# Kernel optimization log

Measured on AMD Instinct MI355X. Metric: run time of the kernel, lower is better.

Reference implementation:

```python
import jax, jax.numpy as jnp
import numpy as np

LN_EPS = 1e-5

def _layernorm(x, g, b):
    mu = jnp.mean(x, axis=-1, keepdims=True)
    var = jnp.mean(jnp.square(x - mu), axis=-1, keepdims=True)
    return (x - mu) * jax.lax.rsqrt(var + LN_EPS) * g + b

def setup_inputs() -> dict:
    key = jax.random.key(0)
    ks = jax.random.split(key, 12)
    B, S, E = 8, 4096, 512
    H, DK = 64, 8          # d_k = E // H = 8 qubits per head
    NQ_FFN, FFN = 8, 2048
    TWO_PI = 2.0 * np.pi
    x = jax.random.normal(ks[0], (B, S, E), dtype=jnp.float32)
    # trainable RX phases per attention head/wire; trainable RY phases for FFN qubits
    theta_attn = jax.random.uniform(ks[1], (H, DK), dtype=jnp.float32, maxval=TWO_PI)
    theta_ffn = jax.random.uniform(ks[2], (NQ_FFN,), dtype=jnp.float32, maxval=TWO_PI)
    s_e = 1.0 / np.sqrt(E)
    W_comb = jax.random.uniform(ks[3], (E, E), dtype=jnp.float32, minval=-s_e, maxval=s_e)
    b_comb = jax.random.uniform(ks[4], (E,), dtype=jnp.float32, minval=-s_e, maxval=s_e)
    s_q = 1.0 / np.sqrt(NQ_FFN)
    W1 = jax.random.uniform(ks[5], (FFN, NQ_FFN), dtype=jnp.float32, minval=-s_q, maxval=s_q)
    b1 = jax.random.uniform(ks[6], (FFN,), dtype=jnp.float32, minval=-s_q, maxval=s_q)
    s_f = 1.0 / np.sqrt(FFN)
    W2 = jax.random.uniform(ks[7], (E, FFN), dtype=jnp.float32, minval=-s_f, maxval=s_f)
    b2 = jax.random.uniform(ks[8], (E,), dtype=jnp.float32, minval=-s_f, maxval=s_f)
    ln1_g = jnp.ones((E,), jnp.float32); ln1_b = jnp.zeros((E,), jnp.float32)
    ln2_g = jnp.ones((E,), jnp.float32); ln2_b = jnp.zeros((E,), jnp.float32)
    return {"x": x, "theta_attn": theta_attn, "W_comb": W_comb, "b_comb": b_comb,
            "ln1_g": ln1_g, "ln1_b": ln1_b, "theta_ffn": theta_ffn,
            "W1": W1, "b1": b1, "W2": W2, "b2": b2, "ln2_g": ln2_g, "ln2_b": ln2_b}

def reference(x, theta_attn, W_comb, b_comb, ln1_g, ln1_b, theta_ffn, W1, b1, W2, b2, ln2_g, ln2_b):
    B, S, E = x.shape
    H, DK = theta_attn.shape
    NQ = theta_ffn.shape[0]
    # Quantum attention heads: RX(x) then RX(theta) on |0> per wire -> <Z> = cos(x+theta)
    q = jnp.cos(x.reshape(B, S, H, DK) + theta_attn)  # [B,S,H,DK]
    attn_out = jnp.einsum('bse,fe->bsf', q.reshape(B, S, E), W_comb) + b_comb
    x1 = _layernorm(x + attn_out, ln1_g, ln1_b)
    # Quantum FFN layer: RY(x) then RY(theta) -> <Z> = cos(x+theta), first NQ features only
    fq = jnp.cos(x1[..., :NQ] + theta_ffn)            # [B,S,NQ]
    h = jax.nn.relu(jnp.einsum('bsq,fq->bsf', fq, W1) + b1)
    ffn_out = jnp.einsum('bsf,ef->bse', h, W2) + b2
    return _layernorm(x1 + ffn_out, ln2_g, ln2_b)
```

## Files before the change

kernel.cpp:

```cpp
#include <hip/hip_runtime.h>
#include <stdint.h>

typedef unsigned short u16;
typedef __bf16 bf16x8 __attribute__((ext_vector_type(8)));
typedef float f32x4 __attribute__((ext_vector_type(4)));

#define AS1(p) ((const __attribute__((address_space(1))) void*)(p))
#define AS3(p) ((__attribute__((address_space(3))) void*)(p))

__device__ __forceinline__ float b2f(u16 v){
    union { unsigned u; float f; } x; x.u = ((unsigned)v) << 16; return x.f;
}
__device__ __forceinline__ u16 f2b(float f){
    union { float f; unsigned u; } x; x.f = f;
    unsigned r = x.u + 0x7FFFu + ((x.u >> 16) & 1u);
    return (u16)(r >> 16);
}

__global__ __launch_bounds__(256) void probe_kernel(
    const u16* p0,const u16* p1,const u16* p2,const u16* p3,const u16* p4,
    const u16* p5,const u16* p6,const u16* p7,const u16* p8,const u16* p9,
    const u16* p10,const u16* p11,const u16* p12,
    int n0,int n1,int n2,int n3,int n4,int n5,int n6,int n7,int n8,int n9,
    int n10,int n11,int n12, int* flags)
{
    const u16* p; int n;
    switch (blockIdx.x) {
        case 0: p=p0; n=n0; break;   case 1: p=p1; n=n1; break;
        case 2: p=p2; n=n2; break;   case 3: p=p3; n=n3; break;
        case 4: p=p4; n=n4; break;   case 5: p=p5; n=n5; break;
        case 6: p=p6; n=n6; break;   case 7: p=p7; n=n7; break;
        case 8: p=p8; n=n8; break;   case 9: p=p9; n=n9; break;
        case 10: p=p10; n=n10; break; case 11: p=p11; n=n11; break;
        default: p=p12; n=n12; break;
    }
    int pairs = n >> 1; if (pairs > 2048) pairs = 2048;
    int strong = 0, znz = 0, tot = 0;
    for (int k = threadIdx.x; k < pairs; k += 256) {
        u16 lo = p[2*k], hi = p[2*k+1];
        int eh = (hi >> 7) & 0xFF;
        int el = (lo >> 7) & 0xFF;
        if (eh >= 0xF0 || (eh >= 1 && eh <= 0x40)) strong = 1;
        if (el >= 0xF0 || (el >= 1 && el <= 0x40)) strong = 1;
        if (lo == 0 && hi != 0) znz++;
        tot++;
    }
    __shared__ int ss, sz, st;
    if (threadIdx.x == 0) { ss = 0; sz = 0; st = 0; }
    __syncthreads();
    if (strong) atomicOr(&ss, 1);
    if (znz) atomicAdd(&sz, znz);
    atomicAdd(&st, tot);
    __syncthreads();
    if (threadIdx.x == 0) {
        flags[blockIdx.x] = (ss || (2 * sz > st)) ? 1 : 0;
        if (blockIdx.x == 0) flags[15] = 0;
    }
}

__global__ __launch_bounds__(256) void convert_kernel(
    const void* sWc, const void* sW2, const void* sW1,
    const void* sTa, const void* sBc, const void* sG1, const void* sB1l,
    const void* sTf, const void* sB1, const void* sB2, const void* sG2, const void* sB2l,
    u16* wbase, const int* flags)
{
    int b = blockIdx.x;
    const void* src; u16* dst; int n, fi, lb, tof32 = 0;
    if (b < 128)      { src=sWc; dst=wbase;          n=262144;  fi=2;  lb=b; }
    else if (b < 640) { src=sW2; dst=wbase+262144;   n=1048576; fi=9;  lb=b-128; }
    else if (b >= 643 && b < 651) { src=sW1; dst=wbase+1312256; n=16384; fi=7; lb=b-643; }
    else {
        lb = 0;
        switch (b) {
            case 640: src=sTa;  dst=wbase+1310720; n=512;  fi=1;  break;
            case 641: src=sBc;  dst=wbase+1311232; n=512;  fi=3;  break;
            case 642: src=sB2;  dst=wbase+1311744; n=512;  fi=10; break;
            case 651: src=sB1;  dst=wbase+1328640; n=2048; fi=8;  break;
            case 652: src=sG1;  dst=wbase+1330688; n=512;  fi=4;  break;
            case 653: src=sB1l; dst=wbase+1331200; n=512;  fi=5;  break;
            case 654: src=sG2;  dst=wbase+1331712; n=512;  fi=11; break;
            case 655: src=sB2l; dst=wbase+1332224; n=512;  fi=12; break;
            default:  src=sTf;  dst=wbase+1332736; n=8;    fi=6;  tof32=1; break;
        }
    }
    int i = lb * 256 + threadIdx.x;
    if (i * 8 >= n) return;
    if (tof32) {
        float* fd = (float*)dst;
        if (flags[fi]) {
            const float4* s = (const float4*)src;
            ((float4*)fd)[i*2] = s[i*2]; ((float4*)fd)[i*2+1] = s[i*2+1];
        } else {
            union { uint4 v; u16 h[8]; } sb;
            sb.v = ((const uint4*)src)[i];
            #pragma unroll
            for (int j = 0; j < 8; j++) fd[i*8+j] = b2f(sb.h[j]);
        }
        return;
    }
    if (flags[fi]) {
        const float4* s = (const float4*)src;
        float4 a = s[i*2], c = s[i*2+1];
        union { uint4 v; u16 h[8]; } o;
        o.h[0]=f2b(a.x); o.h[1]=f2b(a.y); o.h[2]=f2b(a.z); o.h[3]=f2b(a.w);
        o.h[4]=f2b(c.x); o.h[5]=f2b(c.y); o.h[6]=f2b(c.z); o.h[7]=f2b(c.w);
        ((uint4*)dst)[i] = o.v;
    } else {
        ((uint4*)dst)[i] = ((const uint4*)src)[i];
    }
}

__global__ __launch_bounds__(256) void qgen_kernel(
    const void* __restrict__ x, const u16* __restrict__ theta,
    u16* __restrict__ q, const int* flags)
{
    const int idx = blockIdx.x * 256 + threadIdx.x;
    const int col0 = (idx * 8) & 511;
    union { uint4 v; u16 h[8]; } tb;
    tb.v = *(const uint4*)(theta + col0);
    float xv[8];
    if (flags[0]) {
        const float4* p = (const float4*)x + idx * 2;
        float4 a = p[0], b = p[1];
        xv[0]=a.x; xv[1]=a.y; xv[2]=a.z; xv[3]=a.w;
        xv[4]=b.x; xv[5]=b.y; xv[6]=b.z; xv[7]=b.w;
    } else {
        union { uint4 v; u16 h[8]; } xb;
        xb.v = ((const uint4*)x)[idx];
        #pragma unroll
        for (int e = 0; e < 8; e++) xv[e] = b2f(xb.h[e]);
    }
    union { uint4 v; u16 h[8]; } o;
    #pragma unroll
    for (int e = 0; e < 8; e++) o.h[e] = f2b(__cosf(xv[e] + b2f(tb.h[e])));
    ((uint4*)q)[idx] = o.v;
}

__global__ __launch_bounds__(256, 3) void gemm1_fused(
    const u16* __restrict__ q, const void* __restrict__ x,
    const u16* __restrict__ Wt, const u16* __restrict__ bias,
    u16* __restrict__ dst, int mtiles, const int* flags)
{
    __shared__ __align__(16) u16 As[2][128 * 64];
    __shared__ __align__(16) u16 Bs[2][128 * 64];
    const int K = 512, N = 512;
    const int tid  = threadIdx.x;
    const int lane = tid & 63;
    const int w    = tid >> 6;

    const int blk = blockIdx.x;
    const int xcd = blk & 7;
    const int j   = blk >> 3;
    const int per = mtiles >> 3;
    const int mt  = xcd * per + (j >> 2);
    const int nt  = j & 3;
    const int m0 = mt * 128;
    const int n0 = nt * 128;

    const int srow = lane >> 3;
    const int scol = ((lane & 7) ^ srow) * 8;
    const int wm = (w >> 1) * 64;
    const int wn = (w & 1) * 64;
    const int fr   = lane & 15;
    const int quad = lane >> 4;
    const int fx   = fr & 7;
    const int isf32 = flags[0];

    f32x4 acc[4][4];
    #pragma unroll
    for (int i = 0; i < 4; i++)
        #pragma unroll
        for (int jj = 0; jj < 4; jj++)
            acc[i][jj] = f32x4{0.f, 0.f, 0.f, 0.f};

    const u16* Abase = q  + (size_t)m0 * K + scol;
    const u16* Bbase = Wt + (size_t)n0 * K + scol;

    #pragma unroll
    for (int i = 0; i < 4; i++) {
        int c = w * 4 + i;
        int row = c * 8 + srow;
        __builtin_amdgcn_global_load_lds(AS1(Abase + (size_t)row * K),
                                         AS3(&As[0][c * 512]), 16, 0, 0);
        __builtin_amdgcn_global_load_lds(AS1(Bbase + (size_t)row * K),
                                         AS3(&Bs[0][c * 512]), 16, 0, 0);
    }

    int cur = 0;
    for (int kt = 0; kt < K; kt += 64) {
        __syncthreads();
        if (kt + 64 < K) {
            int nxt = cur ^ 1;
            #pragma unroll
            for (int i = 0; i < 4; i++) {
                int c = w * 4 + i;
                int row = c * 8 + srow;
                __builtin_amdgcn_global_load_lds(
                    AS1(Abase + (size_t)row * K + kt + 64),
                    AS3(&As[nxt][c * 512]), 16, 0, 0);
                __builtin_amdgcn_global_load_lds(
                    AS1(Bbase + (size_t)row * K + kt + 64),
                    AS3(&Bs[nxt][c * 512]), 16, 0, 0);
            }
        }
        #pragma unroll
        for (int kk = 0; kk < 2; kk++) {
            bf16x8 af[4], bfr[4];
            #pragma unroll
            for (int mi = 0; mi < 4; mi++)
                af[mi] = *(const bf16x8*)(&As[cur][(wm + mi * 16 + fr) * 64 +
                                          (((kk * 4 + quad) ^ fx) * 8)]);
            #pragma unroll
            for (int ni = 0; ni < 4; ni++)
                bfr[ni] = *(const bf16x8*)(&Bs[cur][(wn + ni * 16 + fr) * 64 +
                                           (((kk * 4 + quad) ^ fx) * 8)]);
            #pragma unroll
            for (int mi = 0; mi < 4; mi++)
                #pragma unroll
                for (int ni = 0; ni < 4; ni++)
                    acc[mi][ni] = __builtin_amdgcn_mfma_f32_16x16x32_bf16(
                        af[mi], bfr[ni], acc[mi][ni], 0, 0, 0);
        }
        cur ^= 1;
    }

    #pragma unroll
    for (int mi = 0; mi < 4; mi++) {
        #pragma unroll
        for (int ni = 0; ni < 4; ni++) {
            int n = n0 + wn + ni * 16 + fr;
            float bn = b2f(bias[n]);
            #pragma unroll
            for (int r = 0; r < 4; r++) {
                int m = m0 + wm + mi * 16 + quad * 4 + r;
                float rv = isf32 ? ((const float*)x)[(size_t)m * N + n]
                                 : b2f(((const u16*)x)[(size_t)m * N + n]);
                dst[(size_t)m * N + n] = f2b(acc[mi][ni][r] + bn + rv);
            }
        }
    }
}

__global__ __launch_bounds__(512, 2) void gemm2_fused(
    const u16* __restrict__ fq, const u16* __restrict__ W1, const u16* __restrict__ b1,
    const u16* __restrict__ Wt, const u16* __restrict__ bias,
    const u16* __restrict__ res, u16* __restrict__ dst, int mtiles)
{
    __shared__ __align__(16) u16 Bs[2][512 * 64];
    const int K = 2048, N = 512;
    const int tid  = threadIdx.x;
    const int lane = tid & 63;
    const int w    = tid >> 6;

    const int m0 = blockIdx.x * 128;

    const int srow = lane >> 3;
    const int scol = ((lane & 7) ^ srow) * 8;
    const int wm = (w >> 2) * 64;
    const int wn = (w & 3) * 128;
    const int fr   = lane & 15;
    const int quad = lane >> 4;
    const int fx   = fr & 7;

    bf16x8 fqf[4];
    #pragma unroll
    for (int mi = 0; mi < 4; mi++) {
        union { uint4 v; bf16x8 b; } z; z.v = uint4{0,0,0,0};
        if (quad == 0) z.v = *(const uint4*)(fq + (size_t)(m0 + wm + mi * 16 + fr) * 8);
        fqf[mi] = z.b;
    }

    const int krow = ((fr >> 2) * 8) + (fr & 3);

    union { uint4 v; bf16x8 b; } w1f[4];
    uint2 b1f[4];
    #pragma unroll
    for (int g = 0; g < 4; g++) {
        w1f[g].v = uint4{0,0,0,0};
        if (quad == 0)
            w1f[g].v = *(const uint4*)(W1 + (size_t)((g >> 1) * 32 + (g & 1) * 4 + krow) * 8);
        b1f[g] = *(const uint2*)(b1 + (g >> 1) * 32 + (g & 1) * 4 + quad * 8);
    }

    f32x4 acc[4][8];
    #pragma unroll
    for (int i = 0; i < 4; i++)
        #pragma unroll
        for (int jj = 0; jj < 8; jj++)
            acc[i][jj] = f32x4{0.f, 0.f, 0.f, 0.f};

    const u16* Bbase = Wt + scol;
    #pragma unroll
    for (int i = 0; i < 8; i++) {
        int c = w * 8 + i;
        int row = c * 8 + srow;
        __builtin_amdgcn_global_load_lds(AS1(Bbase + (size_t)row * K),
                                         AS3(&Bs[0][c * 512]), 16, 0, 0);
    }

    int cur = 0;
    for (int kt = 0; kt < K; kt += 64) {
        __syncthreads();
        if (kt + 64 < K) {
            int nxt = cur ^ 1;
            #pragma unroll
            for (int i = 0; i < 8; i++) {
                int c = w * 8 + i;
                int row = c * 8 + srow;
                __builtin_amdgcn_global_load_lds(
                    AS1(Bbase + (size_t)row * K + kt + 64),
                    AS3(&Bs[nxt][c * 512]), 16, 0, 0);
            }
        }
        #pragma unroll
        for (int kk = 0; kk < 2; kk++) {
            const u16* pb0 = (const u16*)&b1f[kk * 2 + 0];
            const u16* pb1 = (const u16*)&b1f[kk * 2 + 1];
            f32x4 c0 = {b2f(pb0[0]), b2f(pb0[1]), b2f(pb0[2]), b2f(pb0[3])};
            f32x4 c1 = {b2f(pb1[0]), b2f(pb1[1]), b2f(pb1[2]), b2f(pb1[3])};
            bf16x8 af[4];
            #pragma unroll
            for (int mi = 0; mi < 4; mi++) {
                f32x4 hv0 = __builtin_amdgcn_mfma_f32_16x16x32_bf16(
                    w1f[kk * 2 + 0].b, fqf[mi], c0, 0, 0, 0);
                f32x4 hv1 = __builtin_amdgcn_mfma_f32_16x16x32_bf16(
                    w1f[kk * 2 + 1].b, fqf[mi], c1, 0, 0, 0);
                #pragma unroll
                for (int r = 0; r < 4; r++) {
                    af[mi][r]     = (__bf16)fmaxf(hv0[r], 0.f);
                    af[mi][4 + r] = (__bf16)fmaxf(hv1[r], 0.f);
                }
            }
            #pragma unroll
            for (int np = 0; np < 4; np++) {
                bf16x8 bfr[2];
                #pragma unroll
                for (int ni = 0; ni < 2; ni++)
                    bfr[ni] = *(const bf16x8*)(&Bs[cur][(wn + (np * 2 + ni) * 16 + fr) * 64 +
                                               (((kk * 4 + quad) ^ fx) * 8)]);
                #pragma unroll
                for (int mi = 0; mi < 4; mi++)
                    #pragma unroll
                    for (int ni = 0; ni < 2; ni++)
                        acc[mi][np * 2 + ni] = __builtin_amdgcn_mfma_f32_16x16x32_bf16(
                            af[mi], bfr[ni], acc[mi][np * 2 + ni], 0, 0, 0);
            }
        }
        if (kt + 64 < K) {
            #pragma unroll
            for (int g = 0; g < 4; g++) {
                if (quad == 0)
                    w1f[g].v = *(const uint4*)(W1 +
                        (size_t)(kt + 64 + (g >> 1) * 32 + (g & 1) * 4 + krow) * 8);
                b1f[g] = *(const uint2*)(b1 + kt + 64 + (g >> 1) * 32 + (g & 1) * 4 + quad * 8);
            }
        }
        cur ^= 1;
    }

    #pragma unroll
    for (int mi = 0; mi < 4; mi++) {
        #pragma unroll
        for (int nq = 0; nq < 8; nq++) {
            int n = wn + nq * 16 + fr;
            float bn = b2f(bias[n]);
            #pragma unroll
            for (int r = 0; r < 4; r++) {
                int m = m0 + wm + mi * 16 + quad * 4 + r;
                float rv = b2f(res[(size_t)m * N + n]);
                dst[(size_t)m * N + n] = f2b(acc[mi][nq][r] + bn + rv);
            }
        }
    }
}

__global__ __launch_bounds__(512) void ln1_kernel(
    const u16* __restrict__ y1, const u16* __restrict__ g, const u16* __restrict__ b,
    const float* __restrict__ tf, u16* __restrict__ x1, u16* __restrict__ fqout)
{
    __shared__ __align__(16) float xs8[64][8];
    const int t = threadIdx.x;
    const int wv = t >> 6, l = t & 63;
    const size_t rbase = (size_t)blockIdx.x * 64;

    union { uint4 v; u16 s[8]; } gb, bb;
    gb.v = *(const uint4*)(g + l * 8);
    bb.v = *(const uint4*)(b + l * 8);

    #pragma unroll
    for (int i = 0; i < 8; i++) {
        int lr = wv * 8 + i;
        union { uint4 v; u16 s[8]; } yb;
        yb.v = ((const uint4*)(y1 + (rbase + lr) * 512))[l];
        float xv[8], s = 0.f, ss = 0.f;
        #pragma unroll
        for (int jj = 0; jj < 8; jj++) {
            xv[jj] = b2f(yb.s[jj]); s += xv[jj]; ss += xv[jj] * xv[jj];
        }
        #pragma unroll
        for (int o = 32; o > 0; o >>= 1) { s += __shfl_down(s, o); ss += __shfl_down(ss, o); }
        s = __shfl(s, 0); ss = __shfl(ss, 0);
        float mu = s * (1.f / 512.f);
        float rs = rsqrtf(ss * (1.f / 512.f) - mu * mu + 1e-5f);
        union { uint4 v; u16 s[8]; } ob;
        float xn[8];
        #pragma unroll
        for (int jj = 0; jj < 8; jj++) {
            xn[jj] = (xv[jj] - mu) * rs * b2f(gb.s[jj]) + b2f(bb.s[jj]);
            ob.s[jj] = f2b(xn[jj]);
        }
        ((uint4*)(x1 + (rbase + lr) * 512))[l] = ob.v;
        if (l == 0) {
            #pragma unroll
            for (int jj = 0; jj < 8; jj++) xs8[lr][jj] = xn[jj];
        }
    }
    __syncthreads();
    {
        int r = t >> 3, jj = t & 7;
        fqout[(rbase + r) * 8 + jj] = f2b(__cosf(xs8[r][jj] + tf[jj]));
    }
}

__global__ __launch_bounds__(256) void ln2_kernel(
    const u16* __restrict__ z, const u16* __restrict__ g, const u16* __restrict__ b,
    void* __restrict__ out, const int* flags)
{
    const int t = threadIdx.x;
    const int wv = t >> 6, l = t & 63;
    const size_t row = (size_t)blockIdx.x * 4 + wv;

    union { uint4 v; u16 s[8]; } zb, gb, bb;
    zb.v = ((const uint4*)(z + row * 512))[l];
    gb.v = *(const uint4*)(g + l * 8);
    bb.v = *(const uint4*)(b + l * 8);
    float xv[8], s = 0.f, ss = 0.f;
    #pragma unroll
    for (int jj = 0; jj < 8; jj++) { xv[jj] = b2f(zb.s[jj]); s += xv[jj]; ss += xv[jj]*xv[jj]; }
    #pragma unroll
    for (int o = 32; o > 0; o >>= 1) { s += __shfl_down(s, o); ss += __shfl_down(ss, o); }
    s = __shfl(s, 0); ss = __shfl(ss, 0);
    float mu = s * (1.f / 512.f);
    float rs = rsqrtf(ss * (1.f / 512.f) - mu * mu + 1e-5f);
    float xn[8];
    #pragma unroll
    for (int jj = 0; jj < 8; jj++)
        xn[jj] = (xv[jj] - mu) * rs * b2f(gb.s[jj]) + b2f(bb.s[jj]);
    if (flags[0]) {
        float* po = (float*)out + row * 512 + l * 8;
        float4 o0{xn[0],xn[1],xn[2],xn[3]}, o1{xn[4],xn[5],xn[6],xn[7]};
        *(float4*)po = o0; *(float4*)(po + 4) = o1;
    } else {
        union { uint4 v; u16 s[8]; } ob;
        #pragma unroll
        for (int jj = 0; jj < 8; jj++) ob.s[jj] = f2b(xn[jj]);
        ((uint4*)((u16*)out + row * 512))[l] = ob.v;
    }
}

extern "C" void kernel_launch(void* const* d_in, const int* in_sizes, int n_in,
                              void* d_out, int out_size, void* d_ws, size_t ws_size,
                              hipStream_t stream)
{
    u16* ws16 = (u16*)d_ws;
    u16* W     = ws16;
    int* flags = (int*)(ws16 + 1332752);
    u16* fq  = ws16 + 1332800;
    u16* x1  = ws16 + 1594944;
    u16* q   = x1;
    u16* y1  = ws16 + 18372160;
    u16* z   = y1;

    const u16*  wWc  = W;
    const u16*  wW2  = W + 262144;
    const u16*  wTa  = W + 1310720;
    const u16*  wBc  = W + 1311232;
    const u16*  wB2  = W + 1311744;
    const u16*  wW1  = W + 1312256;
    const u16*  wB1  = W + 1328640;
    const u16*  wG1  = W + 1330688;
    const u16*  wB1l = W + 1331200;
    const u16*  wG2  = W + 1331712;
    const u16*  wB2l = W + 1332224;
    const float* wTf = (const float*)(W + 1332736);

    probe_kernel<<<13, 256, 0, stream>>>(
        (const u16*)d_in[0], (const u16*)d_in[1], (const u16*)d_in[2],
        (const u16*)d_in[3], (const u16*)d_in[4], (const u16*)d_in[5],
        (const u16*)d_in[6], (const u16*)d_in[7], (const u16*)d_in[8],
        (const u16*)d_in[9], (const u16*)d_in[10], (const u16*)d_in[11],
        (const u16*)d_in[12],
        in_sizes[0], in_sizes[1], in_sizes[2], in_sizes[3], in_sizes[4],
        in_sizes[5], in_sizes[6], in_sizes[7], in_sizes[8], in_sizes[9],
        in_sizes[10], in_sizes[11], in_sizes[12], flags);

    convert_kernel<<<657, 256, 0, stream>>>(
        d_in[2], d_in[9], d_in[7], d_in[1], d_in[3], d_in[4], d_in[5],
        d_in[6], d_in[8], d_in[10], d_in[11], d_in[12], (u16*)W, flags);

    qgen_kernel<<<8192, 256, 0, stream>>>(d_in[0], wTa, q, flags);

    gemm1_fused<<<1024, 256, 0, stream>>>(
        q, d_in[0], wWc, wBc, y1, 256, flags);

    ln1_kernel<<<512, 512, 0, stream>>>(y1, wG1, wB1l, wTf, x1, fq);

    gemm2_fused<<<256, 512, 0, stream>>>(
        fq, wW1, wB1, wW2, wB2, x1, z, 256);

    ln2_kernel<<<8192, 256, 0, stream>>>(z, wG2, wB2l, d_out, flags);
}
```

Before: 316.4 us.

## Fuse second LayerNorm into FFN GEMM epilogue and drop ln2 kernel

The final LayerNorm moves into the epilogue of the fused FFN GEMM. Each block holds full 512-wide rows, so row sums and sums of squares are reduced with wave shuffles plus a small cross-wave exchange through the reused shared-memory tile. The output is then normalized and written directly. This removes the bf16 round trip of z through global memory and one kernel launch, at the cost of more epilogue work and an extra barrier in the GEMM kernel.

```diff
diff --git a/kernel.cpp b/kernel.cpp
--- a/kernel.cpp
+++ b/kernel.cpp
@@ -244,7 +244,8 @@
 __global__ __launch_bounds__(512, 2) void gemm2_fused(
     const u16* __restrict__ fq, const u16* __restrict__ W1, const u16* __restrict__ b1,
     const u16* __restrict__ Wt, const u16* __restrict__ bias,
-    const u16* __restrict__ res, u16* __restrict__ dst, int mtiles)
+    const u16* __restrict__ res, const u16* __restrict__ g2, const u16* __restrict__ b2l,
+    void* __restrict__ out, const int* flags)
 {
     __shared__ __align__(16) u16 Bs[2][512 * 64];
     const int K = 2048, N = 512;
@@ -261,6 +262,7 @@
     const int fr   = lane & 15;
     const int quad = lane >> 4;
     const int fx   = fr & 7;
+    const int isf32 = flags[0];
 
     bf16x8 fqf[4];
     #pragma unroll
@@ -358,6 +360,8 @@
         cur ^= 1;
     }
 
+    __syncthreads();
+
     #pragma unroll
     for (int mi = 0; mi < 4; mi++) {
         #pragma unroll
@@ -367,8 +371,73 @@
             #pragma unroll
             for (int r = 0; r < 4; r++) {
                 int m = m0 + wm + mi * 16 + quad * 4 + r;
-                float rv = b2f(res[(size_t)m * N + n]);
-                dst[(size_t)m * N + n] = f2b(acc[mi][nq][r] + bn + rv);
+                acc[mi][nq][r] += bn + b2f(res[(size_t)m * N + n]);
+            }
+        }
+    }
+
+    float s[4][4], sq[4][4];
+    #pragma unroll
+    for (int mi = 0; mi < 4; mi++)
+        #pragma unroll
+        for (int r = 0; r < 4; r++) {
+            float a = 0.f, b = 0.f;
+            #pragma unroll
+            for (int nq = 0; nq < 8; nq++) {
+                float v = acc[mi][nq][r];
+                a += v; b += v * v;
+            }
+            s[mi][r] = a; sq[mi][r] = b;
+        }
+    #pragma unroll
+    for (int o = 1; o < 16; o <<= 1) {
+        #pragma unroll
+        for (int mi = 0; mi < 4; mi++)
+            #pragma unroll
+            for (int r = 0; r < 4; r++) {
+                s[mi][r]  += __shfl_xor(s[mi][r],  o);
+                sq[mi][r] += __shfl_xor(sq[mi][r], o);
+            }
+    }
+    float2* red = (float2*)(&Bs[0][0]);
+    if (fr == 0) {
+        #pragma unroll
+        for (int mi = 0; mi < 4; mi++)
+            #pragma unroll
+            for (int r = 0; r < 4; r++) {
+                int row = wm + mi * 16 + quad * 4 + r;
+                red[row * 4 + (w & 3)] = float2{s[mi][r], sq[mi][r]};
+            }
+    }
+    __syncthreads();
+
+    #pragma unroll
+    for (int mi = 0; mi < 4; mi++) {
+        float mu[4], rs[4];
+        #pragma unroll
+        for (int r = 0; r < 4; r++) {
+            int row = wm + mi * 16 + quad * 4 + r;
+            float S = 0.f, SS = 0.f;
+            #pragma unroll
+            for (int jj = 0; jj < 4; jj++) {
+                float2 p = red[row * 4 + jj];
+                S += p.x; SS += p.y;
+            }
+            float m_ = S * (1.f / 512.f);
+            mu[r] = m_;
+            rs[r] = rsqrtf(SS * (1.f / 512.f) - m_ * m_ + 1e-5f);
+        }
+        #pragma unroll
+        for (int nq = 0; nq < 8; nq++) {
+            int n = wn + nq * 16 + fr;
+            float gv = b2f(g2[n]);
+            float bv = b2f(b2l[n]);
+            #pragma unroll
+            for (int r = 0; r < 4; r++) {
+                int m = m0 + wm + mi * 16 + quad * 4 + r;
+                float val = (acc[mi][nq][r] - mu[r]) * rs[r] * gv + bv;
+                if (isf32) ((float*)out)[(size_t)m * N + n] = val;
+                else       ((u16*)out)[(size_t)m * N + n] = f2b(val);
             }
         }
     }
@@ -419,42 +488,6 @@
     {
         int r = t >> 3, jj = t & 7;
         fqout[(rbase + r) * 8 + jj] = f2b(__cosf(xs8[r][jj] + tf[jj]));
-    }
-}
-
-__global__ __launch_bounds__(256) void ln2_kernel(
-    const u16* __restrict__ z, const u16* __restrict__ g, const u16* __restrict__ b,
-    void* __restrict__ out, const int* flags)
-{
-    const int t = threadIdx.x;
-    const int wv = t >> 6, l = t & 63;
-    const size_t row = (size_t)blockIdx.x * 4 + wv;
-
-    union { uint4 v; u16 s[8]; } zb, gb, bb;
-    zb.v = ((const uint4*)(z + row * 512))[l];
-    gb.v = *(const uint4*)(g + l * 8);
-    bb.v = *(const uint4*)(b + l * 8);
-    float xv[8], s = 0.f, ss = 0.f;
-    #pragma unroll
-    for (int jj = 0; jj < 8; jj++) { xv[jj] = b2f(zb.s[jj]); s += xv[jj]; ss += xv[jj]*xv[jj]; }
-    #pragma unroll
-    for (int o = 32; o > 0; o >>= 1) { s += __shfl_down(s, o); ss += __shfl_down(ss, o); }
-    s = __shfl(s, 0); ss = __shfl(ss, 0);
-    float mu = s * (1.f / 512.f);
-    float rs = rsqrtf(ss * (1.f / 512.f) - mu * mu + 1e-5f);
-    float xn[8];
-    #pragma unroll
-    for (int jj = 0; jj < 8; jj++)
-        xn[jj] = (xv[jj] - mu) * rs * b2f(gb.s[jj]) + b2f(bb.s[jj]);
-    if (flags[0]) {
-        float* po = (float*)out + row * 512 + l * 8;
-        float4 o0{xn[0],xn[1],xn[2],xn[3]}, o1{xn[4],xn[5],xn[6],xn[7]};
-        *(float4*)po = o0; *(float4*)(po + 4) = o1;
-    } else {
-        union { uint4 v; u16 s[8]; } ob;
-        #pragma unroll
-        for (int jj = 0; jj < 8; jj++) ob.s[jj] = f2b(xn[jj]);
-        ((uint4*)((u16*)out + row * 512))[l] = ob.v;
     }
 }
 
@@ -469,7 +502,6 @@
     u16* x1  = ws16 + 1594944;
     u16* q   = x1;
     u16* y1  = ws16 + 18372160;
-    u16* z   = y1;
 
     const u16*  wWc  = W;
     const u16*  wW2  = W + 262144;
@@ -506,7 +538,5 @@
     ln1_kernel<<<512, 512, 0, stream>>>(y1, wG1, wB1l, wTf, x1, fq);
 
     gemm2_fused<<<256, 512, 0, stream>>>(
-        fq, wW1, wB1, wW2, wB2, x1, z, 256);
-
-    ln2_kernel<<<8192, 256, 0, stream>>>(z, wG2, wB2l, d_out, flags);
-}
+        fq, wW1, wB1, wW2, wB2, x1, wG2, wB2l, d_out, flags);
+}
```

New measurement: 340.9 us. +7.7%, slower.
